# Performance work log

Measured on AMD Instinct MI355X. Metric: run time of the kernel, lower is better.

Reference implementation:

```python
import jax, jax.numpy as jnp
import numpy as np

NEG_SLOPE = 0.2  # DenseGATConv default negative_slope


def dense_gat(x, adj, W, att_src, att_dst, bias):
    # x: [B,N,Cin], adj: [B,N,N] (self-loops already added), W: [Cin,H*C]
    B, N, _ = x.shape
    H, C = att_src.shape
    h = (x @ W).reshape(B, N, H, C)
    a_src = jnp.einsum('bnhc,hc->bnh', h, att_src)  # [B,N,H]
    a_dst = jnp.einsum('bnhc,hc->bnh', h, att_dst)
    # alpha[b,i,j,h] = a_src[b,j,h] + a_dst[b,i,h]  (softmax over j, axis=2)
    alpha = a_src[:, None, :, :] + a_dst[:, :, None, :]
    alpha = jnp.where(alpha >= 0, alpha, NEG_SLOPE * alpha)  # leaky_relu
    mask = (adj != 0)[..., None]  # [B,N,N,1]
    alpha = jax.nn.softmax(jnp.where(mask, alpha, -1e30), axis=2)
    out = jnp.einsum('bijh,bjhc->bihc', alpha, h).reshape(B, N, H * C)
    return out + bias


def setup_inputs() -> dict:
    key = jax.random.key(0)
    ks = jax.random.split(key, 8)
    B, N, D = 1, 8192, 128
    x = jax.random.normal(ks[0], (B, N, D), dtype=jnp.float32)
    adj = (jax.random.uniform(ks[1], (B, N, N)) < 0.01).astype(jnp.float32)
    idx = jnp.arange(N)
    adj = adj.at[:, idx, idx].set(1.0)  # DenseGATConv add_loop=True
    s = 1.0 / np.sqrt(D)
    lin = lambda k: jax.random.uniform(k, (D, D), minval=-s, maxval=s, dtype=jnp.float32)
    att = lambda k: jax.random.normal(k, (1, D), dtype=jnp.float32) * 0.1  # heads=1
    return dict(
        x=x, adj=adj,
        W0=lin(ks[2]), att_src0=att(ks[3]), att_dst0=att(ks[4]), b0=jnp.zeros((D,), jnp.float32),
        W1=lin(ks[5]), att_src1=att(ks[6]), att_dst1=att(ks[7]), b1=jnp.zeros((D,), jnp.float32),
    )


def reference(x, adj, W0, att_src0, att_dst0, b0, W1, att_src1, att_dst1, b1):
    out0 = dense_gat(x, adj, W0, att_src0, att_dst0, b0)
    out0 = jax.nn.relu(out0)  # relu_layers_index = [0]
    out1 = dense_gat(out0, adj, W1, att_src1, att_dst1, b1)
    # dropout_rate = 0 -> dropout is identity; squeeze batch dim as in block
    return (out0[0], out1[0])
```

## Files before the change

### kernel.cpp

```cpp
#include <hip/hip_runtime.h>

#define MAXDEG 192
#define NEG_SLOPE 0.2f
#define D 128

__device__ __forceinline__ float bf2f(unsigned short u) {
    return __uint_as_float(((unsigned)u) << 16);
}
__device__ __forceinline__ unsigned short f2bf(float f) {
    unsigned u = __float_as_uint(f);
    return (unsigned short)((u + 0x7fffu + ((u >> 16) & 1u)) >> 16);
}

__global__ void detect_dtype(const void* __restrict__ adj, int* __restrict__ flag) {
    if (threadIdx.x == 0)
        *flag = (((const unsigned*)adj)[0] == 0x3F800000u) ? 1 : 0;
}

__global__ __launch_bounds__(256) void build_ell(
        const void* __restrict__ adj, const int* __restrict__ flag,
        unsigned short* __restrict__ cols, int* __restrict__ deg, int N) {
    __shared__ int cnt;
    const int row = blockIdx.x;
    if (threadIdx.x == 0) cnt = 0;
    __syncthreads();
    const int f32m = *flag;
    if (f32m) {
        const float4* arow = (const float4*)((const float*)adj + (size_t)row * N);
        const int nv = N / 4;
        for (int v = threadIdx.x; v < nv; v += 256) {
            float4 u = arow[v];
            const unsigned* uu = (const unsigned*)&u;
            #pragma unroll
            for (int e = 0; e < 4; e++) {
                if (uu[e] != 0u) {
                    int p = atomicAdd(&cnt, 1);
                    if (p < MAXDEG) cols[(size_t)row * MAXDEG + p] = (unsigned short)(v * 4 + e);
                }
            }
        }
    } else {
        const uint4* arow = (const uint4*)((const unsigned short*)adj + (size_t)row * N);
        const int nv = N / 8;
        for (int v = threadIdx.x; v < nv; v += 256) {
            uint4 u = arow[v];
            const unsigned short* us = (const unsigned short*)&u;
            #pragma unroll
            for (int e = 0; e < 8; e++) {
                if (us[e] != 0) {
                    int p = atomicAdd(&cnt, 1);
                    if (p < MAXDEG) cols[(size_t)row * MAXDEG + p] = (unsigned short)(v * 8 + e);
                }
            }
        }
    }
    __syncthreads();
    if (threadIdx.x == 0) deg[row] = cnt < MAXDEG ? cnt : MAXDEG;
}

__global__ __launch_bounds__(256) void gemm128(
        const void* __restrict__ A, const void* __restrict__ W,
        const int* __restrict__ flag, float* __restrict__ H, int a_force_f32) {
    __shared__ float xs[32 * D];
    __shared__ float wsf[64 * D];
    const int tid = threadIdx.x;
    const size_t row0 = (size_t)blockIdx.x * 32;
    const int f32m = *flag;
    const int aF = a_force_f32 | f32m;

    if (aF) {
        const float4* av = (const float4*)((const float*)A + row0 * D);
        float4* xl = (float4*)xs;
        #pragma unroll
        for (int k = 0; k < 4; k++) xl[tid + 256 * k] = av[tid + 256 * k];
    } else {
        const uint4* av = (const uint4*)((const unsigned short*)A + row0 * D);
        #pragma unroll
        for (int k = 0; k < 2; k++) {
            uint4 u = av[tid + 256 * k];
            const unsigned short* us = (const unsigned short*)&u;
            #pragma unroll
            for (int e = 0; e < 8; e++) xs[(tid + 256 * k) * 8 + e] = bf2f(us[e]);
        }
    }

    const int tx = tid & 31, ty = tid >> 5;
    const int c0 = tx * 4, r0 = ty * 4;
    float acc[4][4] = {};
    for (int p = 0; p < 2; p++) {
        __syncthreads();
        if (f32m) {
            const float4* wv = (const float4*)((const float*)W + (size_t)p * 64 * D);
            float4* wl = (float4*)wsf;
            #pragma unroll
            for (int k = 0; k < 8; k++) wl[tid + 256 * k] = wv[tid + 256 * k];
        } else {
            const uint4* wv = (const uint4*)((const unsigned short*)W + (size_t)p * 64 * D);
            #pragma unroll
            for (int k = 0; k < 4; k++) {
                uint4 u = wv[tid + 256 * k];
                const unsigned short* us = (const unsigned short*)&u;
                #pragma unroll
                for (int e = 0; e < 8; e++) wsf[(tid + 256 * k) * 8 + e] = bf2f(us[e]);
            }
        }
        __syncthreads();
        #pragma unroll 8
        for (int k = 0; k < 64; k++) {
            float4 wv = *(const float4*)&wsf[k * D + c0];
            #pragma unroll
            for (int i = 0; i < 4; i++) {
                float xv = xs[(r0 + i) * D + p * 64 + k];
                acc[i][0] += xv * wv.x; acc[i][1] += xv * wv.y;
                acc[i][2] += xv * wv.z; acc[i][3] += xv * wv.w;
            }
        }
    }
    float* Ho = H + row0 * D;
    #pragma unroll
    for (int i = 0; i < 4; i++)
        *(float4*)&Ho[(r0 + i) * D + c0] =
            make_float4(acc[i][0], acc[i][1], acc[i][2], acc[i][3]);
}

__global__ __launch_bounds__(128) void scores128(
        const float* __restrict__ H, const void* __restrict__ attS,
        const void* __restrict__ attD, const int* __restrict__ flag,
        float* __restrict__ asrc, float* __restrict__ adst) {
    const int i = blockIdx.x, c = threadIdx.x;
    const int f32m = *flag;
    const float as_ = f32m ? ((const float*)attS)[c] : bf2f(((const unsigned short*)attS)[c]);
    const float ad_ = f32m ? ((const float*)attD)[c] : bf2f(((const unsigned short*)attD)[c]);
    const float v = H[(size_t)i * D + c];
    float s = v * as_, d = v * ad_;
    #pragma unroll
    for (int off = 32; off > 0; off >>= 1) {
        s += __shfl_down(s, off);
        d += __shfl_down(d, off);
    }
    __shared__ float r[4];
    const int lane = c & 63, wid = c >> 6;
    if (lane == 0) { r[wid] = s; r[2 + wid] = d; }
    __syncthreads();
    if (c == 0) asrc[i] = r[0] + r[1];
    else if (c == 1) adst[i] = r[2] + r[3];
}

__global__ __launch_bounds__(256) void aggregate(
        const float* __restrict__ H,
        const float* __restrict__ asrc, const float* __restrict__ adst,
        const unsigned short* __restrict__ cols, const int* __restrict__ deg,
        const void* __restrict__ bias, const int* __restrict__ flag,
        float* __restrict__ outF, void* __restrict__ outAny,
        size_t elemOff, int relu) {
    __shared__ float sc[MAXDEG];
    __shared__ int   sj[MAXDEG];
    __shared__ float red[256];
    __shared__ float rbuf[4];
    const int i = blockIdx.x, t = threadIdx.x;
    const int d = deg[i];
    const float ai = adst[i];

    float s = -1e30f;
    if (t < d) {
        int j = cols[(size_t)i * MAXDEG + t];
        sj[t] = j;
        float e = asrc[j] + ai;
        s = (e >= 0.f) ? e : NEG_SLOPE * e;
    }
    const int lane = t & 63, wid = t >> 6;
    float m = s;
    #pragma unroll
    for (int off = 32; off > 0; off >>= 1) m = fmaxf(m, __shfl_down(m, off));
    if (lane == 0) rbuf[wid] = m;
    __syncthreads();
    m = fmaxf(fmaxf(rbuf[0], rbuf[1]), fmaxf(rbuf[2], rbuf[3]));
    float p = 0.f;
    if (t < d) { p = __expf(s - m); sc[t] = p; }
    float l = p;
    #pragma unroll
    for (int off = 32; off > 0; off >>= 1) l += __shfl_down(l, off);
    __syncthreads();
    if (lane == 0) rbuf[wid] = l;
    __syncthreads();
    const float invl = 1.f / (rbuf[0] + rbuf[1] + rbuf[2] + rbuf[3]);

    const int c = t & 127, g = t >> 7;
    float a0 = 0.f, a1 = 0.f;
    int k = g;
    for (; k + 2 < d; k += 4) {
        a0 += sc[k]     * H[(size_t)sj[k]     * D + c];
        a1 += sc[k + 2] * H[(size_t)sj[k + 2] * D + c];
    }
    for (; k < d; k += 2) a0 += sc[k] * H[(size_t)sj[k] * D + c];
    red[t] = a0 + a1;
    __syncthreads();
    if (g == 0) {
        const int f32m = *flag;
        const float b = f32m ? ((const float*)bias)[c] : bf2f(((const unsigned short*)bias)[c]);
        float v = (red[c] + red[128 + c]) * invl + b;
        if (relu) v = fmaxf(v, 0.f);
        if (outF) outF[(size_t)i * D + c] = v;
        if (f32m) ((float*)outAny)[elemOff + (size_t)i * D + c] = v;
        else ((unsigned short*)outAny)[elemOff + (size_t)i * D + c] = f2bf(v);
    }
}

extern "C" void kernel_launch(void* const* d_in, const int* in_sizes, int n_in,
                              void* d_out, int out_size, void* d_ws, size_t ws_size,
                              hipStream_t stream) {
    const int N = in_sizes[0] / D;

    char* w = (char*)d_ws;
    int* flag            = (int*)w;            w += 256;
    int* deg             = (int*)w;            w += (size_t)N * sizeof(int);
    unsigned short* cols = (unsigned short*)w; w += (size_t)N * MAXDEG * sizeof(unsigned short);
    float* h             = (float*)w;          w += (size_t)N * D * sizeof(float);
    float* out0          = (float*)w;          w += (size_t)N * D * sizeof(float);
    float* asrc          = (float*)w;          w += (size_t)N * sizeof(float);
    float* adst          = (float*)w;

    detect_dtype<<<1, 64, 0, stream>>>(d_in[1], flag);
    build_ell<<<N, 256, 0, stream>>>(d_in[1], flag, cols, deg, N);

    gemm128<<<N / 32, 256, 0, stream>>>(d_in[0], d_in[2], flag, h, 0);
    scores128<<<N, 128, 0, stream>>>(h, d_in[3], d_in[4], flag, asrc, adst);
    aggregate<<<N, 256, 0, stream>>>(h, asrc, adst, cols, deg, d_in[5], flag,
                                     out0, d_out, 0, 1);

    gemm128<<<N / 32, 256, 0, stream>>>(out0, d_in[6], flag, h, 1);
    scores128<<<N, 128, 0, stream>>>(h, d_in[7], d_in[8], flag, asrc, adst);
    aggregate<<<N, 256, 0, stream>>>(h, asrc, adst, cols, deg, d_in[9], flag,
                                     nullptr, d_out, (size_t)N * D, 0);
}
```

Before: 486.2 us.

## Fuse attention scores into GEMM, use one wavefront per row in ELL build and aggregation

Removes the separate dtype-detect and score kernels: each kernel now checks the adjacency dtype inline, and the GEMM epilogue computes the src/dst attention scores from its accumulators with a 32-lane shuffle reduction. build_ell and aggregate now map one 64-lane wavefront per row, four rows per block. This cuts block count and per-row synchronisation. Aggregation gathers float2 per lane with four independent accumulators, softmax reductions use xor shuffles, and the 1/l normalisation is folded into the stored weights. This targets launch overhead, redundant H re-reads, and the block-wide reductions and barriers, at the cost of fewer threads per row in the gather.

```diff
diff --git a/kernel.cpp b/kernel.cpp
--- a/kernel.cpp
+++ b/kernel.cpp
@@ -11,61 +11,64 @@
     unsigned u = __float_as_uint(f);
     return (unsigned short)((u + 0x7fffu + ((u >> 16) & 1u)) >> 16);
 }
-
-__global__ void detect_dtype(const void* __restrict__ adj, int* __restrict__ flag) {
-    if (threadIdx.x == 0)
-        *flag = (((const unsigned*)adj)[0] == 0x3F800000u) ? 1 : 0;
+__device__ __forceinline__ int is_f32(const void* adj) {
+    return ((const unsigned*)adj)[0] == 0x3F800000u;
 }
 
 __global__ __launch_bounds__(256) void build_ell(
-        const void* __restrict__ adj, const int* __restrict__ flag,
+        const void* __restrict__ adj,
         unsigned short* __restrict__ cols, int* __restrict__ deg, int N) {
-    __shared__ int cnt;
-    const int row = blockIdx.x;
-    if (threadIdx.x == 0) cnt = 0;
+    __shared__ int cnt[4];
+    const int w = threadIdx.x >> 6, lane = threadIdx.x & 63;
+    const int row = blockIdx.x * 4 + w;
+    if (lane == 0) cnt[w] = 0;
     __syncthreads();
-    const int f32m = *flag;
-    if (f32m) {
+    unsigned short* crow = cols + (size_t)row * MAXDEG;
+    if (is_f32(adj)) {
         const float4* arow = (const float4*)((const float*)adj + (size_t)row * N);
         const int nv = N / 4;
-        for (int v = threadIdx.x; v < nv; v += 256) {
-            float4 u = arow[v];
-            const unsigned* uu = (const unsigned*)&u;
-            #pragma unroll
-            for (int e = 0; e < 4; e++) {
-                if (uu[e] != 0u) {
-                    int p = atomicAdd(&cnt, 1);
-                    if (p < MAXDEG) cols[(size_t)row * MAXDEG + p] = (unsigned short)(v * 4 + e);
-                }
-            }
+        for (int v = lane; v < nv; v += 128) {
+            float4 u0 = arow[v];
+            float4 u1 = arow[v + 64];
+            const unsigned* a0 = (const unsigned*)&u0;
+            const unsigned* a1 = (const unsigned*)&u1;
+            #pragma unroll
+            for (int e = 0; e < 4; e++)
+                if (a0[e]) { int p = atomicAdd(&cnt[w], 1); if (p < MAXDEG) crow[p] = (unsigned short)(v * 4 + e); }
+            #pragma unroll
+            for (int e = 0; e < 4; e++)
+                if (a1[e]) { int p = atomicAdd(&cnt[w], 1); if (p < MAXDEG) crow[p] = (unsigned short)((v + 64) * 4 + e); }
         }
     } else {
         const uint4* arow = (const uint4*)((const unsigned short*)adj + (size_t)row * N);
         const int nv = N / 8;
-        for (int v = threadIdx.x; v < nv; v += 256) {
-            uint4 u = arow[v];
-            const unsigned short* us = (const unsigned short*)&u;
-            #pragma unroll
-            for (int e = 0; e < 8; e++) {
-                if (us[e] != 0) {
-                    int p = atomicAdd(&cnt, 1);
-                    if (p < MAXDEG) cols[(size_t)row * MAXDEG + p] = (unsigned short)(v * 8 + e);
-                }
-            }
+        for (int v = lane; v < nv; v += 128) {
+            uint4 u0 = arow[v];
+            uint4 u1 = arow[v + 64];
+            const unsigned short* s0 = (const unsigned short*)&u0;
+            const unsigned short* s1 = (const unsigned short*)&u1;
+            #pragma unroll
+            for (int e = 0; e < 8; e++)
+                if (s0[e]) { int p = atomicAdd(&cnt[w], 1); if (p < MAXDEG) crow[p] = (unsigned short)(v * 8 + e); }
+            #pragma unroll
+            for (int e = 0; e < 8; e++)
+                if (s1[e]) { int p = atomicAdd(&cnt[w], 1); if (p < MAXDEG) crow[p] = (unsigned short)((v + 64) * 8 + e); }
         }
     }
     __syncthreads();
-    if (threadIdx.x == 0) deg[row] = cnt < MAXDEG ? cnt : MAXDEG;
+    if (lane == 0) deg[row] = cnt[w] < MAXDEG ? cnt[w] : MAXDEG;
 }
 
 __global__ __launch_bounds__(256) void gemm128(
         const void* __restrict__ A, const void* __restrict__ W,
-        const int* __restrict__ flag, float* __restrict__ H, int a_force_f32) {
+        const void* __restrict__ adjFlag, float* __restrict__ H,
+        const void* __restrict__ attS, const void* __restrict__ attD,
+        float* __restrict__ asrc, float* __restrict__ adst, int a_force_f32) {
     __shared__ float xs[32 * D];
     __shared__ float wsf[64 * D];
     const int tid = threadIdx.x;
     const size_t row0 = (size_t)blockIdx.x * 32;
-    const int f32m = *flag;
+    const int f32m = is_f32(adjFlag);
     const int aF = a_force_f32 | f32m;
 
     if (aF) {
@@ -121,88 +124,101 @@
     for (int i = 0; i < 4; i++)
         *(float4*)&Ho[(r0 + i) * D + c0] =
             make_float4(acc[i][0], acc[i][1], acc[i][2], acc[i][3]);
-}
-
-__global__ __launch_bounds__(128) void scores128(
-        const float* __restrict__ H, const void* __restrict__ attS,
-        const void* __restrict__ attD, const int* __restrict__ flag,
-        float* __restrict__ asrc, float* __restrict__ adst) {
-    const int i = blockIdx.x, c = threadIdx.x;
-    const int f32m = *flag;
-    const float as_ = f32m ? ((const float*)attS)[c] : bf2f(((const unsigned short*)attS)[c]);
-    const float ad_ = f32m ? ((const float*)attD)[c] : bf2f(((const unsigned short*)attD)[c]);
-    const float v = H[(size_t)i * D + c];
-    float s = v * as_, d = v * ad_;
-    #pragma unroll
-    for (int off = 32; off > 0; off >>= 1) {
-        s += __shfl_down(s, off);
-        d += __shfl_down(d, off);
-    }
-    __shared__ float r[4];
-    const int lane = c & 63, wid = c >> 6;
-    if (lane == 0) { r[wid] = s; r[2 + wid] = d; }
-    __syncthreads();
-    if (c == 0) asrc[i] = r[0] + r[1];
-    else if (c == 1) adst[i] = r[2] + r[3];
+
+    float aSv[4], aDv[4];
+    #pragma unroll
+    for (int j = 0; j < 4; j++) {
+        aSv[j] = f32m ? ((const float*)attS)[c0 + j] : bf2f(((const unsigned short*)attS)[c0 + j]);
+        aDv[j] = f32m ? ((const float*)attD)[c0 + j] : bf2f(((const unsigned short*)attD)[c0 + j]);
+    }
+    #pragma unroll
+    for (int i = 0; i < 4; i++) {
+        float s = acc[i][0] * aSv[0] + acc[i][1] * aSv[1] + acc[i][2] * aSv[2] + acc[i][3] * aSv[3];
+        float d = acc[i][0] * aDv[0] + acc[i][1] * aDv[1] + acc[i][2] * aDv[2] + acc[i][3] * aDv[3];
+        #pragma unroll
+        for (int off = 16; off > 0; off >>= 1) {
+            s += __shfl_down(s, off, 32);
+            d += __shfl_down(d, off, 32);
+        }
+        if (tx == 0) {
+            asrc[row0 + r0 + i] = s;
+            adst[row0 + r0 + i] = d;
+        }
+    }
 }
 
 __global__ __launch_bounds__(256) void aggregate(
         const float* __restrict__ H,
         const float* __restrict__ asrc, const float* __restrict__ adst,
         const unsigned short* __restrict__ cols, const int* __restrict__ deg,
-        const void* __restrict__ bias, const int* __restrict__ flag,
+        const void* __restrict__ bias, const void* __restrict__ adjFlag,
         float* __restrict__ outF, void* __restrict__ outAny,
         size_t elemOff, int relu) {
-    __shared__ float sc[MAXDEG];
-    __shared__ int   sj[MAXDEG];
-    __shared__ float red[256];
-    __shared__ float rbuf[4];
-    const int i = blockIdx.x, t = threadIdx.x;
+    __shared__ float scn[4][MAXDEG];
+    __shared__ unsigned short sjj[4][MAXDEG];
+    const int w = threadIdx.x >> 6, lane = threadIdx.x & 63;
+    const int i = blockIdx.x * 4 + w;
     const int d = deg[i];
     const float ai = adst[i];
-
-    float s = -1e30f;
-    if (t < d) {
-        int j = cols[(size_t)i * MAXDEG + t];
-        sj[t] = j;
-        float e = asrc[j] + ai;
-        s = (e >= 0.f) ? e : NEG_SLOPE * e;
-    }
-    const int lane = t & 63, wid = t >> 6;
-    float m = s;
-    #pragma unroll
-    for (int off = 32; off > 0; off >>= 1) m = fmaxf(m, __shfl_down(m, off));
-    if (lane == 0) rbuf[wid] = m;
+    const unsigned short* crow = cols + (size_t)i * MAXDEG;
+
+    const int s0 = lane, s1 = lane + 64, s2 = lane + 128;
+    unsigned short j0 = 0, j1 = 0, j2 = 0;
+    float e0 = -3e38f, e1 = -3e38f, e2 = -3e38f;
+    if (s0 < d) { j0 = crow[s0]; float e = asrc[j0] + ai; e0 = (e >= 0.f) ? e : NEG_SLOPE * e; }
+    if (s1 < d) { j1 = crow[s1]; float e = asrc[j1] + ai; e1 = (e >= 0.f) ? e : NEG_SLOPE * e; }
+    if (s2 < d) { j2 = crow[s2]; float e = asrc[j2] + ai; e2 = (e >= 0.f) ? e : NEG_SLOPE * e; }
+    float m = fmaxf(e0, fmaxf(e1, e2));
+    #pragma unroll
+    for (int off = 1; off < 64; off <<= 1) m = fmaxf(m, __shfl_xor(m, off));
+    float p0 = (s0 < d) ? __expf(e0 - m) : 0.f;
+    float p1 = (s1 < d) ? __expf(e1 - m) : 0.f;
+    float p2 = (s2 < d) ? __expf(e2 - m) : 0.f;
+    float l = p0 + p1 + p2;
+    #pragma unroll
+    for (int off = 1; off < 64; off <<= 1) l += __shfl_xor(l, off);
+    const float invl = 1.f / l;
+    scn[w][s0] = p0 * invl; sjj[w][s0] = j0;
+    scn[w][s1] = p1 * invl; sjj[w][s1] = j1;
+    scn[w][s2] = p2 * invl; sjj[w][s2] = j2;
     __syncthreads();
-    m = fmaxf(fmaxf(rbuf[0], rbuf[1]), fmaxf(rbuf[2], rbuf[3]));
-    float p = 0.f;
-    if (t < d) { p = __expf(s - m); sc[t] = p; }
-    float l = p;
-    #pragma unroll
-    for (int off = 32; off > 0; off >>= 1) l += __shfl_down(l, off);
-    __syncthreads();
-    if (lane == 0) rbuf[wid] = l;
-    __syncthreads();
-    const float invl = 1.f / (rbuf[0] + rbuf[1] + rbuf[2] + rbuf[3]);
-
-    const int c = t & 127, g = t >> 7;
-    float a0 = 0.f, a1 = 0.f;
-    int k = g;
-    for (; k + 2 < d; k += 4) {
-        a0 += sc[k]     * H[(size_t)sj[k]     * D + c];
-        a1 += sc[k + 2] * H[(size_t)sj[k + 2] * D + c];
-    }
-    for (; k < d; k += 2) a0 += sc[k] * H[(size_t)sj[k] * D + c];
-    red[t] = a0 + a1;
-    __syncthreads();
-    if (g == 0) {
-        const int f32m = *flag;
-        const float b = f32m ? ((const float*)bias)[c] : bf2f(((const unsigned short*)bias)[c]);
-        float v = (red[c] + red[128 + c]) * invl + b;
-        if (relu) v = fmaxf(v, 0.f);
-        if (outF) outF[(size_t)i * D + c] = v;
-        if (f32m) ((float*)outAny)[elemOff + (size_t)i * D + c] = v;
-        else ((unsigned short*)outAny)[elemOff + (size_t)i * D + c] = f2bf(v);
+
+    const float2* H2 = (const float2*)H;
+    float2 a0 = {0.f, 0.f}, a1 = {0.f, 0.f}, a2 = {0.f, 0.f}, a3 = {0.f, 0.f};
+    int k = 0;
+    for (; k + 3 < d; k += 4) {
+        const int ja = sjj[w][k], jb = sjj[w][k + 1], jc = sjj[w][k + 2], jd = sjj[w][k + 3];
+        const float wa = scn[w][k], wb = scn[w][k + 1], wc = scn[w][k + 2], wd = scn[w][k + 3];
+        const float2 va = H2[(size_t)ja * 64 + lane];
+        const float2 vb = H2[(size_t)jb * 64 + lane];
+        const float2 vc = H2[(size_t)jc * 64 + lane];
+        const float2 vd = H2[(size_t)jd * 64 + lane];
+        a0.x += wa * va.x; a0.y += wa * va.y;
+        a1.x += wb * vb.x; a1.y += wb * vb.y;
+        a2.x += wc * vc.x; a2.y += wc * vc.y;
+        a3.x += wd * vd.x; a3.y += wd * vd.y;
+    }
+    for (; k < d; k++) {
+        const int j = sjj[w][k];
+        const float wk = scn[w][k];
+        const float2 v = H2[(size_t)j * 64 + lane];
+        a0.x += wk * v.x; a0.y += wk * v.y;
+    }
+    float vx = a0.x + a1.x + a2.x + a3.x;
+    float vy = a0.y + a1.y + a2.y + a3.y;
+
+    const int f32m = is_f32(adjFlag);
+    const int c0 = lane * 2;
+    const float b0 = f32m ? ((const float*)bias)[c0]     : bf2f(((const unsigned short*)bias)[c0]);
+    const float b1 = f32m ? ((const float*)bias)[c0 + 1] : bf2f(((const unsigned short*)bias)[c0 + 1]);
+    vx += b0; vy += b1;
+    if (relu) { vx = fmaxf(vx, 0.f); vy = fmaxf(vy, 0.f); }
+    if (outF) ((float2*)outF)[(size_t)i * 64 + lane] = make_float2(vx, vy);
+    if (f32m) {
+        ((float2*)outAny)[(elemOff >> 1) + (size_t)i * 64 + lane] = make_float2(vx, vy);
+    } else {
+        unsigned packed = (unsigned)f2bf(vx) | ((unsigned)f2bf(vy) << 16);
+        ((unsigned*)outAny)[(elemOff >> 1) + (size_t)i * 64 + lane] = packed;
     }
 }
 
@@ -212,7 +228,6 @@
     const int N = in_sizes[0] / D;
 
     char* w = (char*)d_ws;
-    int* flag            = (int*)w;            w += 256;
     int* deg             = (int*)w;            w += (size_t)N * sizeof(int);
     unsigned short* cols = (unsigned short*)w; w += (size_t)N * MAXDEG * sizeof(unsigned short);
     float* h             = (float*)w;          w += (size_t)N * D * sizeof(float);
@@ -220,16 +235,17 @@
     float* asrc          = (float*)w;          w += (size_t)N * sizeof(float);
     float* adst          = (float*)w;
 
-    detect_dtype<<<1, 64, 0, stream>>>(d_in[1], flag);
-    build_ell<<<N, 256, 0, stream>>>(d_in[1], flag, cols, deg, N);
-
-    gemm128<<<N / 32, 256, 0, stream>>>(d_in[0], d_in[2], flag, h, 0);
-    scores128<<<N, 128, 0, stream>>>(h, d_in[3], d_in[4], flag, asrc, adst);
-    aggregate<<<N, 256, 0, stream>>>(h, asrc, adst, cols, deg, d_in[5], flag,
-                                     out0, d_out, 0, 1);
-
-    gemm128<<<N / 32, 256, 0, stream>>>(out0, d_in[6], flag, h, 1);
-    scores128<<<N, 128, 0, stream>>>(h, d_in[7], d_in[8], flag, asrc, adst);
-    aggregate<<<N, 256, 0, stream>>>(h, asrc, adst, cols, deg, d_in[9], flag,
-                                     nullptr, d_out, (size_t)N * D, 0);
-}
+    const void* adj = d_in[1];
+
+    build_ell<<<N / 4, 256, 0, stream>>>(adj, cols, deg, N);
+
+    gemm128<<<N / 32, 256, 0, stream>>>(d_in[0], d_in[2], adj, h,
+                                        d_in[3], d_in[4], asrc, adst, 0);
+    aggregate<<<N / 4, 256, 0, stream>>>(h, asrc, adst, cols, deg, d_in[5], adj,
+                                         out0, d_out, 0, 1);
+
+    gemm128<<<N / 32, 256, 0, stream>>>(out0, d_in[6], adj, h,
+                                        d_in[7], d_in[8], asrc, adst, 1);
+    aggregate<<<N / 4, 256, 0, stream>>>(h, asrc, adst, cols, deg, d_in[9], adj,
+                                         nullptr, d_out, (size_t)N * D, 0);
+}
```

Measured after the change: 459.0 us. 5.6% less time.
